# Kernel tuning notes

Hardware: AMD Instinct MI355X
Metric: run time of the kernel (lower is better)

The kernel has to match this reference:

```python
import jax, jax.numpy as jnp
import numpy as np

B, S, D, H = 4, 2048, 1024, 16
HD = D // H


def setup_inputs() -> dict:
    key = jax.random.key(0)
    kx, kq, kk, kv, ko = jax.random.split(key, 5)
    scale = np.float32(1.0 / np.sqrt(D))
    return {
        "x": jax.random.normal(kx, (B, S, D), dtype=jnp.float32),
        "attention_mask": jnp.ones((B, S), dtype=jnp.int32),
        "Wq": jax.random.normal(kq, (D, D), dtype=jnp.float32) * scale,
        "Wk": jax.random.normal(kk, (D, D), dtype=jnp.float32) * scale,
        "Wv": jax.random.normal(kv, (D, D), dtype=jnp.float32) * scale,
        "Wo": jax.random.normal(ko, (D, D), dtype=jnp.float32) * scale,
    }


def reference(x, attention_mask, Wq, Wk, Wv, Wo):
    b, s, d = x.shape
    h, hd = H, d // H
    # project and split heads: [b, h, s, hd]
    q = (x @ Wq).reshape(b, s, h, hd).transpose(0, 2, 1, 3)
    k = (x @ Wk).reshape(b, s, h, hd).transpose(0, 2, 1, 3)
    v = (x @ Wv).reshape(b, s, h, hd).transpose(0, 2, 1, 3)
    inv_sqrt_hd = np.float32(1.0 / np.sqrt(hd))
    score = jnp.einsum("bhqd,bhkd->bhqk", q, k) * inv_sqrt_hd  # [b,h,s,s]
    idx = jnp.arange(s)
    causal_mask = (idx[None, :] <= idx[:, None])[None, None]  # [1,1,s,s]
    key_mask = attention_mask.astype(bool)[:, None, None, :]  # [b,1,1,s]
    score = jnp.where(causal_mask & key_mask, score, -jnp.inf)
    attn = jax.nn.softmax(score, axis=-1)
    out = jnp.einsum("bhqk,bhkd->bhqd", attn, v)  # [b,h,s,hd]
    out = out.transpose(0, 2, 1, 3).reshape(b, s, d)
    return out @ Wo
```

## Files before the change

kernel.cpp:

```cpp
#include <hip/hip_runtime.h>

typedef __attribute__((ext_vector_type(8))) short short8;
typedef __attribute__((ext_vector_type(4))) float floatx4;
typedef __attribute__((address_space(3))) void lvoid;
typedef const __attribute__((address_space(1))) void gvoid;

#define LOG2E 1.44269504088896340736f

__device__ __forceinline__ ushort f2bf(float f) {
  union { float f; unsigned u; } v; v.f = f;
  unsigned r = v.u + 0x7fffu + ((v.u >> 16) & 1u);
  return (ushort)(r >> 16);
}

__device__ __forceinline__ void gld16(const void* g, void* l) {
  __builtin_amdgcn_global_load_lds((gvoid*)g, (lvoid*)l, 16, 0, 0);
}

__global__ __launch_bounds__(256) void k_prep_x(const float* __restrict__ X,
                                                ushort* __restrict__ Xb) {
  const size_t i = ((size_t)blockIdx.x * 256 + threadIdx.x) * 8;
  float4 v0 = *(const float4*)(X + i);
  float4 v1 = *(const float4*)(X + i + 4);
  ushort u[8] = {f2bf(v0.x), f2bf(v0.y), f2bf(v0.z), f2bf(v0.w),
                 f2bf(v1.x), f2bf(v1.y), f2bf(v1.z), f2bf(v1.w)};
  *(uint4*)(Xb + i) = *(uint4*)u;
}

__global__ __launch_bounds__(256) void k_prep_wt(
    const float* __restrict__ W0, const float* __restrict__ W1,
    const float* __restrict__ W2, const float* __restrict__ W3,
    ushort* __restrict__ T0, ushort* __restrict__ T1,
    ushort* __restrict__ T2, ushort* __restrict__ T3) {
  __shared__ ushort T[64][66];
  const int z = blockIdx.z;
  const float* W = z == 0 ? W0 : (z == 1 ? W1 : (z == 2 ? W2 : W3));
  ushort* Wt = z == 0 ? T0 : (z == 1 ? T1 : (z == 2 ? T2 : T3));
  const int kb = blockIdx.x * 64, nb = blockIdx.y * 64;
  const int t = threadIdx.x, r = t >> 2, c0 = (t & 3) * 16;
  const float* src = W + (size_t)(kb + r) * 1024 + nb + c0;
  #pragma unroll
  for (int i = 0; i < 4; i++) {
    float4 a = ((const float4*)src)[i];
    T[r][c0 + i*4 + 0] = f2bf(a.x); T[r][c0 + i*4 + 1] = f2bf(a.y);
    T[r][c0 + i*4 + 2] = f2bf(a.z); T[r][c0 + i*4 + 3] = f2bf(a.w);
  }
  __syncthreads();
  ushort u[16];
  #pragma unroll
  for (int j = 0; j < 16; j++) u[j] = T[c0 + j][r];
  ushort* dst = Wt + (size_t)(nb + r) * 1024 + kb + c0;
  ((uint4*)dst)[0] = ((uint4*)u)[0];
  ((uint4*)dst)[1] = ((uint4*)u)[1];
}

#define GEMM_LOOP(Aptr, BTptr, BFptr)                                          \
  constexpr int LDB = PREPPED ? 32 : 40;                                       \
  __shared__ __align__(16) ushort As[128 * 32];                                \
  __shared__ __align__(16) ushort Bs[128 * LDB];                               \
  const int tid = threadIdx.x, l = tid & 63, w = tid >> 6;                     \
  const int wm = w >> 1, wn = w & 1, lr = l & 15, lk = l >> 4;                 \
  const int m0 = blockIdx.y * 128, n0 = blockIdx.x * 128;                      \
  const int srow = l >> 2;                                                     \
  const int scol = ((l & 3) ^ ((l >> 3) & 3)) * 8;                             \
  const int c0 = w * 2;                                                        \
  const int xchunk = (lk ^ ((lr >> 1) & 3)) * 8;                               \
  const int bk = tid >> 3, bn = (tid & 7) * 16;                                \
  floatx4 acc[4][4] = {};                                                      \
  for (int kt = 0; kt < 1024; kt += 32) {                                      \
    __syncthreads();                                                           \
    _Pragma("unroll")                                                          \
    for (int i = 0; i < 2; i++) {                                              \
      const int c = c0 + i;                                                    \
      gld16(Aptr + (size_t)(m0 + c*16 + srow) * 1024 + kt + scol, &As[c*512]); \
      if constexpr (PREPPED)                                                   \
        gld16(BTptr + (size_t)(n0 + c*16 + srow) * 1024 + kt + scol,           \
              &Bs[c*512]);                                                     \
    }                                                                          \
    if constexpr (!PREPPED) {                                                  \
      const float* src = BFptr + (size_t)(kt + bk) * 1024 + n0 + bn;           \
      float vb[16];                                                            \
      _Pragma("unroll")                                                        \
      for (int i = 0; i < 4; i++) ((float4*)vb)[i] = ((const float4*)src)[i];  \
      _Pragma("unroll")                                                        \
      for (int i = 0; i < 16; i++) Bs[(bn + i) * 40 + bk] = f2bf(vb[i]);       \
    }                                                                          \
    __syncthreads();                                                           \
    short8 af[4], bfr[4];                                                      \
    _Pragma("unroll")                                                          \
    for (int f = 0; f < 4; f++) {                                              \
      af[f] = *(const short8*)&As[(wm*64 + f*16 + lr) * 32 + xchunk];          \
      if constexpr (PREPPED)                                                   \
        bfr[f] = *(const short8*)&Bs[(wn*64 + f*16 + lr) * 32 + xchunk];       \
      else                                                                     \
        bfr[f] = *(const short8*)&Bs[(wn*64 + f*16 + lr) * 40 + lk*8];         \
    }                                                                          \
    _Pragma("unroll")                                                          \
    for (int i = 0; i < 4; i++)                                                \
      _Pragma("unroll")                                                        \
      for (int j = 0; j < 4; j++)                                              \
        acc[i][j] = __builtin_amdgcn_mfma_f32_16x16x32_bf16(af[i], bfr[j],     \
                                                            acc[i][j], 0,0,0);\
  }

template <bool PREPPED>
__global__ __launch_bounds__(256) void k_proj(
    const ushort* __restrict__ Xb,
    const ushort* __restrict__ Wtq, const ushort* __restrict__ Wtk,
    const ushort* __restrict__ Wtv,
    const float* __restrict__ Wfq, const float* __restrict__ Wfk,
    const float* __restrict__ Wfv,
    ushort* __restrict__ Qo, ushort* __restrict__ Ko, ushort* __restrict__ Vo)
{
  const int z = blockIdx.z;
  const ushort* Bt = PREPPED ? (z == 0 ? Wtq : (z == 1 ? Wtk : Wtv)) : nullptr;
  const float*  Bf = PREPPED ? nullptr : (z == 0 ? Wfq : (z == 1 ? Wfk : Wfv));
  ushort* Out = z == 0 ? Qo : (z == 1 ? Ko : Vo);
  const float scale = z == 0 ? 0.125f : 1.0f;
  GEMM_LOOP(Xb, Bt, Bf)
  if (z == 2) {
    #pragma unroll
    for (int i = 0; i < 4; i++) {
      const int m = m0 + wm*64 + i*16 + lk*4;
      const int bb = m >> 11, s = m & 2047;
      #pragma unroll
      for (int j = 0; j < 4; j++) {
        const int n = n0 + wn*64 + j*16 + lr;
        const int h = n >> 6, hd = n & 63;
        ushort u4[4];
        #pragma unroll
        for (int r = 0; r < 4; r++) u4[r] = f2bf(acc[i][j][r]);
        *(uint2*)(Out + (((size_t)(bb*16 + h)) * 64 + hd) * 2048 + s) = *(uint2*)u4;
      }
    }
  } else {
    #pragma unroll
    for (int i = 0; i < 4; i++) {
      #pragma unroll
      for (int j = 0; j < 4; j++) {
        const int n = n0 + wn*64 + j*16 + lr;
        const int h = n >> 6, hd = n & 63;
        #pragma unroll
        for (int r = 0; r < 4; r++) {
          const int m = m0 + wm*64 + i*16 + lk*4 + r;
          const int bb = m >> 11, s = m & 2047;
          Out[(((size_t)(bb*16 + h)) * 2048 + s) * 64 + hd] = f2bf(acc[i][j][r] * scale);
        }
      }
    }
  }
}

template <bool PREPPED>
__global__ __launch_bounds__(256) void k_out(
    const ushort* __restrict__ A, const ushort* __restrict__ Wt,
    const float* __restrict__ Wf, float* __restrict__ Out)
{
  GEMM_LOOP(A, Wt, Wf)
  #pragma unroll
  for (int i = 0; i < 4; i++) {
    #pragma unroll
    for (int j = 0; j < 4; j++) {
      const int n = n0 + wn*64 + j*16 + lr;
      #pragma unroll
      for (int r = 0; r < 4; r++) {
        const int m = m0 + wm*64 + i*16 + lk*4 + r;
        Out[(size_t)m * 1024 + n] = acc[i][j][r];
      }
    }
  }
}

__global__ __launch_bounds__(256) void k_attn(
    const ushort* __restrict__ Q, const ushort* __restrict__ K,
    const ushort* __restrict__ V, const int* __restrict__ amask,
    ushort* __restrict__ AO)
{
  __shared__ __align__(16) ushort Kl[64 * 64];
  __shared__ __align__(16) ushort Vl[64 * 64];
  __shared__ __align__(16) ushort Pl[4][16 * 72];

  const int tid = threadIdx.x, l = tid & 63, w = tid >> 6;
  const int lr = l & 15, lk = l >> 4;
  const int g = blockIdx.x;
  const int swz = (g & 7) * 128 + (g >> 3);
  const int p = swz & 15, bh = swz >> 4;
  const int b = bh >> 4, h = bh & 15;
  const int qA0 = p * 64, qB0 = (31 - p) * 64;

  const ushort* Qbh = Q + (size_t)bh * 2048 * 64;
  const ushort* Kbh = K + (size_t)bh * 2048 * 64;
  const ushort* Vbh = V + (size_t)bh * 64 * 2048;

  const int qrA = qA0 + w*16 + lr, qrB = qB0 + w*16 + lr;
  short8 aqA0 = *(const short8*)(Qbh + (size_t)qrA * 64 + lk*8);
  short8 aqA1 = *(const short8*)(Qbh + (size_t)qrA * 64 + 32 + lk*8);
  short8 aqB0 = *(const short8*)(Qbh + (size_t)qrB * 64 + lk*8);
  short8 aqB1 = *(const short8*)(Qbh + (size_t)qrB * 64 + 32 + lk*8);

  floatx4 oA[4] = {}, oB[4] = {};
  float mA[4] = {-1e30f,-1e30f,-1e30f,-1e30f}, lA[4] = {};
  float mB[4] = {-1e30f,-1e30f,-1e30f,-1e30f}, lB[4] = {};

  const int krow = l >> 3;
  const int kcol = ((l & 7) ^ krow) * 8;

  const int kend = 31 - p;
  const int amb = b * 2048;
  int kv0 = 0;

  auto process = [&](const short8& q0f, const short8& q1f, floatx4* o,
                     float* mm, float* ll, int qbase, bool diag,
                     const float* kadd) {
    floatx4 sa[4] = {};
    #pragma unroll
    for (int f = 0; f < 4; f++) {
      const int rb = f*16 + lr;
      const int cs = (rb & 7) * 8;
      short8 b0 = *(const short8*)&Kl[rb*64 + ((lk*8) ^ cs)];
      short8 b1 = *(const short8*)&Kl[rb*64 + (((4+lk)*8) ^ cs)];
      sa[f] = __builtin_amdgcn_mfma_f32_16x16x32_bf16(q0f, b0, sa[f], 0,0,0);
      sa[f] = __builtin_amdgcn_mfma_f32_16x16x32_bf16(q1f, b1, sa[f], 0,0,0);
    }
    #pragma unroll
    for (int f = 0; f < 4; f++) {
      const int kv = kv0 + f*16 + lr;
      #pragma unroll
      for (int r = 0; r < 4; r++) {
        sa[f][r] += kadd[f];
        if (diag) {
          const int qq = qbase + w*16 + lk*4 + r;
          if (kv > qq) sa[f][r] = -1e30f;
        }
      }
    }
    float scl[4];
    #pragma unroll
    for (int r = 0; r < 4; r++) {
      float mx = fmaxf(fmaxf(sa[0][r], sa[1][r]), fmaxf(sa[2][r], sa[3][r]));
      mx = fmaxf(mx, __shfl_xor(mx, 1, 64));
      mx = fmaxf(mx, __shfl_xor(mx, 2, 64));
      mx = fmaxf(mx, __shfl_xor(mx, 4, 64));
      mx = fmaxf(mx, __shfl_xor(mx, 8, 64));
      const float mnew = fmaxf(mm[r], mx);
      scl[r] = exp2f((mm[r] - mnew) * LOG2E);
      mm[r] = mnew;
    }
    float rsum[4] = {};
    #pragma unroll
    for (int f = 0; f < 4; f++)
      #pragma unroll
      for (int r = 0; r < 4; r++) {
        float pv = exp2f((sa[f][r] - mm[r]) * LOG2E);
        sa[f][r] = pv;
        rsum[r] += pv;
      }
    #pragma unroll
    for (int r = 0; r < 4; r++) {
      rsum[r] += __shfl_xor(rsum[r], 1, 64);
      rsum[r] += __shfl_xor(rsum[r], 2, 64);
      rsum[r] += __shfl_xor(rsum[r], 4, 64);
      rsum[r] += __shfl_xor(rsum[r], 8, 64);
      ll[r] = ll[r] * scl[r] + rsum[r];
    }
    #pragma unroll
    for (int f = 0; f < 4; f++)
      #pragma unroll
      for (int r = 0; r < 4; r++) o[f][r] *= scl[r];

    #pragma unroll
    for (int r = 0; r < 4; r++) {
      unsigned pk01, pk23;
      asm("v_cvt_pk_bf16_f32 %0, %1, %2" : "=v"(pk01)
          : "v"(sa[0][r]), "v"(sa[1][r]));
      asm("v_cvt_pk_bf16_f32 %0, %1, %2" : "=v"(pk23)
          : "v"(sa[2][r]), "v"(sa[3][r]));
      ushort* prow = &Pl[w][(lk*4 + r) * 72];
      prow[lr]      = (ushort)pk01;
      prow[16 + lr] = (ushort)(pk01 >> 16);
      prow[32 + lr] = (ushort)pk23;
      prow[48 + lr] = (ushort)(pk23 >> 16);
    }
    asm volatile("s_waitcnt lgkmcnt(0)" ::: "memory");
    __builtin_amdgcn_sched_barrier(0);
    short8 ap0 = *(const short8*)&Pl[w][lr*72 + lk*8];
    short8 ap1 = *(const short8*)&Pl[w][lr*72 + 32 + lk*8];
    #pragma unroll
    for (int f = 0; f < 4; f++) {
      const int rb = f*16 + lr;
      const int cs = (rb & 7) * 8;
      short8 bv0 = *(const short8*)&Vl[rb*64 + ((lk*8) ^ cs)];
      short8 bv1 = *(const short8*)&Vl[rb*64 + (((4+lk)*8) ^ cs)];
      o[f] = __builtin_amdgcn_mfma_f32_16x16x32_bf16(ap0, bv0, o[f], 0,0,0);
      o[f] = __builtin_amdgcn_mfma_f32_16x16x32_bf16(ap1, bv1, o[f], 0,0,0);
    }
  };

  for (int t = 0; t <= kend; t++) {
    kv0 = t * 64;
    float kadd[4];
    #pragma unroll
    for (int f = 0; f < 4; f++)
      kadd[f] = amask[amb + kv0 + f*16 + lr] ? 0.f : -1e30f;
    __syncthreads();
    #pragma unroll
    for (int i = 0; i < 2; i++) {
      const int c = w*2 + i;
      gld16(Kbh + (size_t)(kv0 + c*8 + krow) * 64 + kcol, &Kl[c*512]);
      gld16(Vbh + (size_t)(c*8 + krow) * 2048 + kv0 + kcol, &Vl[c*512]);
    }
    __syncthreads();
    process(aqB0, aqB1, oB, mB, lB, qB0, t == kend, kadd);
    if (t <= p) process(aqA0, aqA1, oA, mA, lA, qA0, t == p, kadd);
  }

  #pragma unroll
  for (int r = 0; r < 4; r++) {
    const float invA = lA[r] > 0.f ? 1.0f / lA[r] : 0.f;
    const float invB = lB[r] > 0.f ? 1.0f / lB[r] : 0.f;
    const int sA = qA0 + w*16 + lk*4 + r;
    const int sB = qB0 + w*16 + lk*4 + r;
    const size_t baseA = ((size_t)b * 2048 + sA) * 1024 + h * 64;
    const size_t baseB = ((size_t)b * 2048 + sB) * 1024 + h * 64;
    #pragma unroll
    for (int f = 0; f < 4; f++) {
      AO[baseA + f*16 + lr] = f2bf(oA[f][r] * invA);
      AO[baseB + f*16 + lr] = f2bf(oB[f][r] * invB);
    }
  }
}

extern "C" void kernel_launch(void* const* d_in, const int* in_sizes, int n_in,
                              void* d_out, int out_size, void* d_ws, size_t ws_size,
                              hipStream_t stream) {
  const float* x     = (const float*)d_in[0];
  const int*   amask = (const int*)d_in[1];
  const float* Wq    = (const float*)d_in[2];
  const float* Wk    = (const float*)d_in[3];
  const float* Wv    = (const float*)d_in[4];
  const float* Wo    = (const float*)d_in[5];
  float* out = (float*)d_out;

  const size_t NEL = (size_t)4 * 2048 * 1024;
  const size_t WEL = (size_t)1024 * 1024;

  dim3 blk(256);
  const bool prepped = ws_size >= (size_t)76 * 1024 * 1024;

  if (prepped) {
    ushort* Xb  = (ushort*)d_ws;
    ushort* Wtq = Xb + NEL;
    ushort* Wtk = Wtq + WEL;
    ushort* Wtv = Wtk + WEL;
    ushort* Wto = Wtv + WEL;
    ushort* Qb  = Wto + WEL;
    ushort* Kb  = Qb + NEL;
    ushort* Vb  = Kb + NEL;
    ushort* AO  = Xb;

    k_prep_x<<<4096, blk, 0, stream>>>(x, Xb);
    k_prep_wt<<<dim3(16, 16, 4), blk, 0, stream>>>(Wq, Wk, Wv, Wo,
                                                   Wtq, Wtk, Wtv, Wto);
    k_proj<true><<<dim3(8, 64, 3), blk, 0, stream>>>(
        Xb, Wtq, Wtk, Wtv, nullptr, nullptr, nullptr, Qb, Kb, Vb);
    k_attn<<<dim3(1024), blk, 0, stream>>>(Qb, Kb, Vb, amask, AO);
    k_out<true><<<dim3(8, 64), blk, 0, stream>>>(AO, Wto, nullptr, out);
  } else {
    ushort* Xb = (ushort*)d_ws;
    ushort* Qb = Xb + NEL;
    ushort* Kb = Qb + NEL;
    ushort* Vb = Kb + NEL;
    ushort* AO = Xb;

    k_prep_x<<<4096, blk, 0, stream>>>(x, Xb);
    k_proj<false><<<dim3(8, 64, 3), blk, 0, stream>>>(
        Xb, nullptr, nullptr, nullptr, Wq, Wk, Wv, Qb, Kb, Vb);
    k_attn<<<dim3(1024), blk, 0, stream>>>(Qb, Kb, Vb, amask, AO);
    k_out<false><<<dim3(8, 64), blk, 0, stream>>>(AO, nullptr, Wo, out);
  }
}
```

Before: 363.6 us.

## Transpose QK^T MFMA so each lane owns a query row, add lazy rescale

Swaps the operands of the score MFMA so each lane holds one query's scores in registers. Row max and sum then need two cross-lane shuffles instead of four per row, and the softmax state shrinks to one scalar per lane. It skips the output rescale when the max has not grown by more than 8, uses an FMA-based exp2, and writes P to LDS as packed 64-bit stores. The attention mask is loaded once per tile with a wave-wide all-valid fast path; the cost is extra shuffles to redistribute scale and normalisation factors.

```diff
diff --git a/kernel.cpp b/kernel.cpp
--- a/kernel.cpp
+++ b/kernel.cpp
@@ -199,8 +199,7 @@
   short8 aqB1 = *(const short8*)(Qbh + (size_t)qrB * 64 + 32 + lk*8);
 
   floatx4 oA[4] = {}, oB[4] = {};
-  float mA[4] = {-1e30f,-1e30f,-1e30f,-1e30f}, lA[4] = {};
-  float mB[4] = {-1e30f,-1e30f,-1e30f,-1e30f}, lB[4] = {};
+  float mmA = -1e30f, llA = 0.f, mmB = -1e30f, llB = 0.f;
 
   const int krow = l >> 3;
   const int kcol = ((l & 7) ^ krow) * 8;
@@ -210,76 +209,74 @@
   int kv0 = 0;
 
   auto process = [&](const short8& q0f, const short8& q1f, floatx4* o,
-                     float* mm, float* ll, int qbase, bool diag,
-                     const float* kadd) {
+                     float& mm, float& ll, int qbase, bool diag,
+                     float mval, bool allv) {
     floatx4 sa[4] = {};
     #pragma unroll
     for (int f = 0; f < 4; f++) {
       const int rb = f*16 + lr;
       const int cs = (rb & 7) * 8;
-      short8 b0 = *(const short8*)&Kl[rb*64 + ((lk*8) ^ cs)];
-      short8 b1 = *(const short8*)&Kl[rb*64 + (((4+lk)*8) ^ cs)];
-      sa[f] = __builtin_amdgcn_mfma_f32_16x16x32_bf16(q0f, b0, sa[f], 0,0,0);
-      sa[f] = __builtin_amdgcn_mfma_f32_16x16x32_bf16(q1f, b1, sa[f], 0,0,0);
-    }
+      short8 k0 = *(const short8*)&Kl[rb*64 + ((lk*8) ^ cs)];
+      short8 k1 = *(const short8*)&Kl[rb*64 + (((4+lk)*8) ^ cs)];
+      sa[f] = __builtin_amdgcn_mfma_f32_16x16x32_bf16(k0, q0f, sa[f], 0,0,0);
+      sa[f] = __builtin_amdgcn_mfma_f32_16x16x32_bf16(k1, q1f, sa[f], 0,0,0);
+    }
+    if (!allv) {
+      #pragma unroll
+      for (int f = 0; f < 4; f++)
+        #pragma unroll
+        for (int r = 0; r < 4; r++)
+          sa[f][r] += __shfl(mval, f*16 + lk*4 + r, 64);
+    }
+    if (diag) {
+      const int q = qbase + w*16 + lr;
+      #pragma unroll
+      for (int f = 0; f < 4; f++)
+        #pragma unroll
+        for (int r = 0; r < 4; r++)
+          if (kv0 + f*16 + lk*4 + r > q) sa[f][r] = -1e30f;
+    }
+    float mx = sa[0][0];
+    #pragma unroll
+    for (int f = 0; f < 4; f++)
+      #pragma unroll
+      for (int r = 0; r < 4; r++) mx = fmaxf(mx, sa[f][r]);
+    mx = fmaxf(mx, __shfl_xor(mx, 16, 64));
+    mx = fmaxf(mx, __shfl_xor(mx, 32, 64));
+    if (!__all(mx <= mm + 8.f)) {
+      const float pm = fmaxf(mm, mx);
+      const float scl = __builtin_exp2f((mm - pm) * LOG2E);
+      mm = pm;
+      ll *= scl;
+      float sclo[4];
+      #pragma unroll
+      for (int r = 0; r < 4; r++) sclo[r] = __shfl(scl, lk*4 + r, 64);
+      #pragma unroll
+      for (int f = 0; f < 4; f++)
+        #pragma unroll
+        for (int r = 0; r < 4; r++) o[f][r] *= sclo[r];
+    }
+    const float nm = mm * LOG2E;
+    float rs = 0.f;
+    #pragma unroll
+    for (int f = 0; f < 4; f++)
+      #pragma unroll
+      for (int r = 0; r < 4; r++) {
+        float pv = __builtin_exp2f(__builtin_fmaf(sa[f][r], LOG2E, -nm));
+        sa[f][r] = pv;
+        rs += pv;
+      }
+    rs += __shfl_xor(rs, 16, 64);
+    rs += __shfl_xor(rs, 32, 64);
+    ll += rs;
     #pragma unroll
     for (int f = 0; f < 4; f++) {
-      const int kv = kv0 + f*16 + lr;
-      #pragma unroll
-      for (int r = 0; r < 4; r++) {
-        sa[f][r] += kadd[f];
-        if (diag) {
-          const int qq = qbase + w*16 + lk*4 + r;
-          if (kv > qq) sa[f][r] = -1e30f;
-        }
-      }
-    }
-    float scl[4];
-    #pragma unroll
-    for (int r = 0; r < 4; r++) {
-      float mx = fmaxf(fmaxf(sa[0][r], sa[1][r]), fmaxf(sa[2][r], sa[3][r]));
-      mx = fmaxf(mx, __shfl_xor(mx, 1, 64));
-      mx = fmaxf(mx, __shfl_xor(mx, 2, 64));
-      mx = fmaxf(mx, __shfl_xor(mx, 4, 64));
-      mx = fmaxf(mx, __shfl_xor(mx, 8, 64));
-      const float mnew = fmaxf(mm[r], mx);
-      scl[r] = exp2f((mm[r] - mnew) * LOG2E);
-      mm[r] = mnew;
-    }
-    float rsum[4] = {};
-    #pragma unroll
-    for (int f = 0; f < 4; f++)
-      #pragma unroll
-      for (int r = 0; r < 4; r++) {
-        float pv = exp2f((sa[f][r] - mm[r]) * LOG2E);
-        sa[f][r] = pv;
-        rsum[r] += pv;
-      }
-    #pragma unroll
-    for (int r = 0; r < 4; r++) {
-      rsum[r] += __shfl_xor(rsum[r], 1, 64);
-      rsum[r] += __shfl_xor(rsum[r], 2, 64);
-      rsum[r] += __shfl_xor(rsum[r], 4, 64);
-      rsum[r] += __shfl_xor(rsum[r], 8, 64);
-      ll[r] = ll[r] * scl[r] + rsum[r];
-    }
-    #pragma unroll
-    for (int f = 0; f < 4; f++)
-      #pragma unroll
-      for (int r = 0; r < 4; r++) o[f][r] *= scl[r];
-
-    #pragma unroll
-    for (int r = 0; r < 4; r++) {
-      unsigned pk01, pk23;
-      asm("v_cvt_pk_bf16_f32 %0, %1, %2" : "=v"(pk01)
-          : "v"(sa[0][r]), "v"(sa[1][r]));
-      asm("v_cvt_pk_bf16_f32 %0, %1, %2" : "=v"(pk23)
-          : "v"(sa[2][r]), "v"(sa[3][r]));
-      ushort* prow = &Pl[w][(lk*4 + r) * 72];
-      prow[lr]      = (ushort)pk01;
-      prow[16 + lr] = (ushort)(pk01 >> 16);
-      prow[32 + lr] = (ushort)pk23;
-      prow[48 + lr] = (ushort)(pk23 >> 16);
+      unsigned pk0, pk1;
+      asm("v_cvt_pk_bf16_f32 %0, %1, %2" : "=v"(pk0)
+          : "v"(sa[f][0]), "v"(sa[f][1]));
+      asm("v_cvt_pk_bf16_f32 %0, %1, %2" : "=v"(pk1)
+          : "v"(sa[f][2]), "v"(sa[f][3]));
+      *(uint2*)&Pl[w][lr*72 + f*16 + lk*4] = make_uint2(pk0, pk1);
     }
     asm volatile("s_waitcnt lgkmcnt(0)" ::: "memory");
     __builtin_amdgcn_sched_barrier(0);
@@ -298,10 +295,9 @@
 
   for (int t = 0; t <= kend; t++) {
     kv0 = t * 64;
-    float kadd[4];
-    #pragma unroll
-    for (int f = 0; f < 4; f++)
-      kadd[f] = amask[amb + kv0 + f*16 + lr] ? 0.f : -1e30f;
+    const int am = amask[amb + kv0 + l];
+    const bool allv = __all(am != 0);
+    const float mval = am ? 0.f : -1e30f;
     __syncthreads();
     #pragma unroll
     for (int i = 0; i < 2; i++) {
@@ -310,22 +306,28 @@
       gld16(Vbh + (size_t)(c*8 + krow) * 2048 + kv0 + kcol, &Vl[c*512]);
     }
     __syncthreads();
-    process(aqB0, aqB1, oB, mB, lB, qB0, t == kend, kadd);
-    if (t <= p) process(aqA0, aqA1, oA, mA, lA, qA0, t == p, kadd);
-  }
-
+    process(aqB0, aqB1, oB, mmB, llB, qB0, t == kend, mval, allv);
+    if (t <= p) process(aqA0, aqA1, oA, mmA, llA, qA0, t == p, mval, allv);
+  }
+
+  const float invA = llA > 0.f ? 1.0f / llA : 0.f;
+  const float invB = llB > 0.f ? 1.0f / llB : 0.f;
+  float ivA[4], ivB[4];
   #pragma unroll
   for (int r = 0; r < 4; r++) {
-    const float invA = lA[r] > 0.f ? 1.0f / lA[r] : 0.f;
-    const float invB = lB[r] > 0.f ? 1.0f / lB[r] : 0.f;
+    ivA[r] = __shfl(invA, lk*4 + r, 64);
+    ivB[r] = __shfl(invB, lk*4 + r, 64);
+  }
+  #pragma unroll
+  for (int r = 0; r < 4; r++) {
     const int sA = qA0 + w*16 + lk*4 + r;
     const int sB = qB0 + w*16 + lk*4 + r;
     const size_t baseA = ((size_t)b * 2048 + sA) * 1024 + h * 64;
     const size_t baseB = ((size_t)b * 2048 + sB) * 1024 + h * 64;
     #pragma unroll
     for (int f = 0; f < 4; f++) {
-      AO[baseA + f*16 + lr] = f2bf(oA[f][r] * invA);
-      AO[baseB + f*16 + lr] = f2bf(oB[f][r] * invB);
+      AO[baseA + f*16 + lr] = f2bf(oA[f][r] * ivA[r]);
+      AO[baseB + f*16 + lr] = f2bf(oB[f][r] * ivB[r]);
     }
   }
 }
```

New measurement: 309.9 us. -14.8%, faster.
